# Optimization experiments

Hardware: AMD Instinct MI355X
Metric: run time of the kernel (lower is better)

## Reference

```python
import jax, jax.numpy as jnp
import numpy as np

N, E, T, H, D_IN, D_OUT = 50000, 320000, 4, 4, 128, 128
NEG_SLOPE = 0.2
LN_EPS = 1e-5


def setup_inputs() -> dict:
    key = jax.random.key(0)
    ks = jax.random.split(key, 10)
    x = jax.random.normal(ks[0], (N, D_IN), jnp.float32)
    edge_index = jax.random.randint(ks[1], (2, E), 0, N, jnp.int32)
    edge_attr = jax.random.randint(ks[2], (E,), 0, T, jnp.int32)
    W_gat = jax.random.normal(ks[3], (T, D_IN, H * D_OUT), jnp.float32) / np.sqrt(D_IN)
    a_src = jax.random.normal(ks[4], (T, H, D_OUT), jnp.float32) / np.sqrt(D_OUT)
    a_dst = jax.random.normal(ks[5], (T, H, D_OUT), jnp.float32) / np.sqrt(D_OUT)
    b_gat = jnp.zeros((T, D_OUT), jnp.float32)
    edge_type_weights = jnp.ones((T,), jnp.float32) / T
    W_fuse = jax.random.normal(ks[6], (T * D_OUT, D_OUT), jnp.float32) / np.sqrt(T * D_OUT)
    b_fuse = jnp.zeros((D_OUT,), jnp.float32)
    ln_gamma = jnp.ones((D_OUT,), jnp.float32)
    ln_beta = jnp.zeros((D_OUT,), jnp.float32)
    return {"x": x, "edge_index": edge_index, "edge_attr": edge_attr,
            "W_gat": W_gat, "a_src": a_src, "a_dst": a_dst, "b_gat": b_gat,
            "edge_type_weights": edge_type_weights, "W_fuse": W_fuse,
            "b_fuse": b_fuse, "ln_gamma": ln_gamma, "ln_beta": ln_beta}


def _gat_one_type(x, src_all, dst_all, mask_all, W, a_s, a_d, b):
    # x: [N, D_in]; src_all/dst_all: [E+N] (type-mask + self-loops on all nodes)
    n = x.shape[0]
    h = (x @ W).reshape(n, H, D_OUT)                      # [N, H, D]
    alpha_s = jnp.sum(h * a_s, axis=-1)                   # [N, H]
    alpha_d = jnp.sum(h * a_d, axis=-1)                   # [N, H]
    logit = jax.nn.leaky_relu(alpha_s[src_all] + alpha_d[dst_all], NEG_SLOPE)  # [Ea, H]
    neg_inf = jnp.float32(-1e30)
    logit = jnp.where(mask_all[:, None], logit, neg_inf)
    m = jax.ops.segment_max(logit, dst_all, num_segments=n)   # [N, H] (self-loops ensure finite)
    ex = jnp.exp(logit - m[dst_all])
    ex = jnp.where(mask_all[:, None], ex, 0.0)
    denom = jax.ops.segment_sum(ex, dst_all, num_segments=n)  # [N, H]
    alpha = ex / denom[dst_all]                                # [Ea, H]
    msg = alpha[:, :, None] * h[src_all]                       # [Ea, H, D]
    out = jax.ops.segment_sum(msg, dst_all, num_segments=n)   # [N, H, D]
    return out.mean(axis=1) + b                                # concat=False -> head mean


def reference(x, edge_index, edge_attr, W_gat, a_src, a_dst, b_gat,
              edge_type_weights, W_fuse, b_fuse, ln_gamma, ln_beta):
    n = x.shape[0]
    self_idx = jnp.arange(n, dtype=edge_index.dtype)
    src_all = jnp.concatenate([edge_index[0], self_idx])
    dst_all = jnp.concatenate([edge_index[1], self_idx])
    outs = []
    for t in range(T):
        mask_all = jnp.concatenate([edge_attr == t, jnp.ones((n,), bool)])
        outs.append(_gat_one_type(x, src_all, dst_all, mask_all,
                                  W_gat[t], a_src[t], a_dst[t], b_gat[t]))
    w = jax.nn.softmax(edge_type_weights)
    x_cat = jnp.concatenate([outs[t] * w[t] for t in range(T)], axis=1)  # [N, T*D]
    y = x_cat @ W_fuse + b_fuse
    mu = jnp.mean(y, axis=-1, keepdims=True)
    var = jnp.var(y, axis=-1, keepdims=True)
    y = (y - mu) / jnp.sqrt(var + LN_EPS) * ln_gamma + ln_beta
    return jax.nn.relu(y)
```

## Files before the change

### kernel.cpp

```cpp
#include <hip/hip_runtime.h>
#include <hip/hip_bf16.h>

#define TT 4
#define HH 4
#define DD 128
#define KAGG 2048

typedef __attribute__((ext_vector_type(8))) short short8;
typedef __attribute__((ext_vector_type(4))) float f32x4;
typedef __attribute__((ext_vector_type(4))) unsigned int uint4v;

__device__ __forceinline__ float lrelu(float z) { return z > 0.f ? z : 0.2f * z; }
__device__ __forceinline__ float bf2f(unsigned short u) {
  union { unsigned int i; float f; } v; v.i = ((unsigned int)u) << 16; return v.f;
}
__device__ __forceinline__ unsigned short f2b(float f) {
  union { float f; unsigned int i; } u; u.f = f;
  unsigned int r = u.i + 0x7fff + ((u.i >> 16) & 1);
  return (unsigned short)(r >> 16);
}
__device__ __forceinline__ void unpack8v(uint4v u, float* hv) {
  hv[0] = bf2f((unsigned short)(u.x & 0xffff));
  hv[1] = bf2f((unsigned short)(u.x >> 16));
  hv[2] = bf2f((unsigned short)(u.y & 0xffff));
  hv[3] = bf2f((unsigned short)(u.y >> 16));
  hv[4] = bf2f((unsigned short)(u.z & 0xffff));
  hv[5] = bf2f((unsigned short)(u.z >> 16));
  hv[6] = bf2f((unsigned short)(u.w & 0xffff));
  hv[7] = bf2f((unsigned short)(u.w >> 16));
}

__global__ __launch_bounds__(256) void prologue_kernel(
    const float* __restrict__ x, unsigned short* __restrict__ xb, int total4,
    const float* __restrict__ Wg, const float* __restrict__ a_s,
    const float* __restrict__ a_d, const float* __restrict__ W_fuse,
    const float* __restrict__ b_gat, const float* __restrict__ etw,
    const float* __restrict__ b_fuse, unsigned short* __restrict__ Pall,
    float* __restrict__ cbias, const int* __restrict__ dst,
    const int* __restrict__ attr, int* __restrict__ deg, int E, int N) {
  int bid = blockIdx.x;
  const int nconv = (total4 + 255) >> 8;
  if (bid < nconv) {
    int i = bid * 256 + threadIdx.x;
    if (i < total4) {
      float4 v = ((const float4*)x)[i];
      ushort4 o;
      o.x = f2b(v.x); o.y = f2b(v.y); o.z = f2b(v.z); o.w = f2b(v.w);
      ((ushort4*)xb)[i] = o;
    }
    return;
  }
  bid -= nconv;
  if (bid < 17) {
    float e0 = etw[0], e1 = etw[1], e2 = etw[2], e3 = etw[3];
    float mx = fmaxf(fmaxf(e0, e1), fmaxf(e2, e3));
    float w0 = __expf(e0 - mx), w1 = __expf(e1 - mx), w2 = __expf(e2 - mx),
          w3 = __expf(e3 - mx);
    float inv = 1.f / (w0 + w1 + w2 + w3);
    float wts[4] = {w0 * inv, w1 * inv, w2 * inv, w3 * inv};
    if (bid < 16) {
      int idx = bid * 256 + threadIdx.x;
      int c = idx >> 7, k = idx & 127;
      int t = c >> 3, jj = c & 7, head = jj & 3;
      const float* av = ((jj < 4) ? a_s : a_d) + (t * 4 + head) * 128;
      const float* wr = Wg + (size_t)t * 65536 + k * 512 + head * 128;
      float s = 0.f;
      for (int m = 0; m < 128; ++m) s += wr[m] * av[m];
      Pall[c * 128 + k] = f2b(s);
    } else {
      int j = threadIdx.x;
      if (j < 128) {
        float s = b_fuse[j];
        for (int t = 0; t < 4; ++t) {
          float st = 0.f;
          for (int m = 0; m < 128; ++m)
            st += b_gat[t * 128 + m] * W_fuse[(size_t)(t * 128 + m) * 128 + j];
          s += wts[t] * st;
        }
        cbias[j] = s;
      }
    }
    return;
  }
  bid -= 17;
  int e = bid * 256 + threadIdx.x;
  if (e < E) atomicAdd(&deg[attr[e] * N + dst[e]], 1);
}

__global__ __launch_bounds__(256) void stage2_kernel(
    const int* __restrict__ deg, int* __restrict__ rowptr,
    int* __restrict__ cursor, int* __restrict__ gcur, int M,
    const float* __restrict__ Wg, const float* __restrict__ W_fuse,
    const float* __restrict__ etw, unsigned short* __restrict__ Gfrag,
    const unsigned short* __restrict__ xb, const unsigned short* __restrict__ Pall,
    float* __restrict__ as_, float* __restrict__ ad_, int N) {
  __shared__ __align__(16) unsigned char smem[65536 + 16];
  int bid = blockIdx.x;
  const int nscan = (M + 255) >> 8;
  if (bid < nscan) {
    int* sh = (int*)smem;
    int* basep = (int*)(smem + 65536);
    int i = bid * 256 + threadIdx.x;
    int v = (i < M) ? deg[i] : 0;
    sh[threadIdx.x] = v;
    __syncthreads();
    for (int off = 1; off < 256; off <<= 1) {
      int xx = (threadIdx.x >= off) ? sh[threadIdx.x - off] : 0;
      __syncthreads();
      sh[threadIdx.x] += xx;
      __syncthreads();
    }
    if (threadIdx.x == 255) *basep = atomicAdd(gcur, sh[255]);
    __syncthreads();
    if (i < M) {
      int r = *basep + sh[threadIdx.x] - v;
      rowptr[i] = r;
      cursor[i] = r;
    }
    return;
  }
  bid -= nscan;
  if (bid < 256) {
    float(*Bs)[128] = (float(*)[128])smem;
    int t = bid >> 6;
    int kr0 = (bid & 63) * 8;
    const float* wf = W_fuse + (size_t)t * 16384;
#pragma unroll
    for (int i = 0; i < 64; ++i)
      ((float*)Bs)[i * 256 + threadIdx.x] = wf[i * 256 + threadIdx.x];

    float e0 = etw[0], e1 = etw[1], e2 = etw[2], e3 = etw[3];
    float mx = fmaxf(fmaxf(e0, e1), fmaxf(e2, e3));
    float w0 = __expf(e0 - mx), w1 = __expf(e1 - mx), w2 = __expf(e2 - mx),
          w3 = __expf(e3 - mx);
    float inv = 1.f / (w0 + w1 + w2 + w3);
    float wt = ((t == 0) ? w0 : (t == 1) ? w1 : (t == 2) ? w2 : w3) * inv * 0.25f;
    __syncthreads();

    int rr = threadIdx.x >> 7;
    int j = threadIdx.x & 127;
#pragma unroll
    for (int r2 = 0; r2 < 4; ++r2) {
      int kr = kr0 + r2 * 2 + rr;
      int head = kr >> 7, k = kr & 127;
      const float* wr = Wg + (size_t)t * 65536 + k * 512 + head * 128;
      float s = 0.f;
      for (int m = 0; m < 128; ++m) s += wr[m] * Bs[m][j];
      s *= wt;
      int K = t * 512 + kr;
      int kt = K >> 7, kk = (K >> 5) & 3, n = j >> 4;
      int f = (kt * 4 + kk) * 8 + n;
      int lg = (K >> 3) & 3, lr = j & 15, j8 = K & 7;
      Gfrag[(size_t)f * 512 + (lg * 16 + lr) * 8 + j8] = f2b(s);
    }
    return;
  }
  bid -= 256;
  unsigned char* lds = smem;
  const int n0 = bid * 128;
  const int tid = threadIdx.x, lane = tid & 63, wid = tid >> 6;
  const int lr = lane & 15, lg = lane >> 4;
#pragma unroll
  for (int i = 0; i < 8; ++i) {
    int chunk = tid + i * 256;
    int row = chunk >> 4, k16 = chunk & 15;
    int gr = n0 + row;
    uint4 v = make_uint4(0, 0, 0, 0);
    if (gr < N) v = *(const uint4*)(xb + (size_t)gr * DD + k16 * 8);
    *(uint4*)(lds + ((row * 256 + k16 * 16) ^ ((row & 7) << 4))) = v;
  }
  __syncthreads();
  f32x4 acc[2][2] = {};
#pragma unroll
  for (int kk = 0; kk < 4; ++kk) {
    short8 a[2], b[2];
#pragma unroll
    for (int m = 0; m < 2; ++m) {
      int row = wid * 32 + m * 16 + lr;
      a[m] = *(const short8*)(lds + ((row * 256 + kk * 64 + (lg << 4)) ^ ((row & 7) << 4)));
    }
#pragma unroll
    for (int n = 0; n < 2; ++n) {
      int c = n * 16 + lr;
      b[n] = *(const short8*)(Pall + c * DD + kk * 32 + lg * 8);
    }
#pragma unroll
    for (int m = 0; m < 2; ++m)
#pragma unroll
      for (int n = 0; n < 2; ++n)
        acc[m][n] = __builtin_amdgcn_mfma_f32_16x16x32_bf16(a[m], b[n], acc[m][n], 0, 0, 0);
  }
#pragma unroll
  for (int m = 0; m < 2; ++m)
#pragma unroll
    for (int n = 0; n < 2; ++n) {
      int c = n * 16 + lr;
      int t = c >> 3, jj = c & 7, head = jj & 3;
      float* dstp = (jj & 4) ? ad_ : as_;
#pragma unroll
      for (int r = 0; r < 4; ++r) {
        int gr = n0 + wid * 32 + m * 16 + lg * 4 + r;
        if (gr < N) dstp[((size_t)t * N + gr) * 4 + head] = acc[m][n][r];
      }
    }
}

__global__ __launch_bounds__(256) void scatter_q_kernel(
    const int* __restrict__ src, const int* __restrict__ dst,
    const int* __restrict__ attr, int* __restrict__ cursor,
    int* __restrict__ slist, float* __restrict__ qlist,
    const float* __restrict__ as_, const float* __restrict__ ad_,
    int E, int N) {
  int e = blockIdx.x * 256 + threadIdx.x;
  if (e >= E) return;
  int t = attr[e], s = src[e], d = dst[e];
  int p = atomicAdd(&cursor[(size_t)t * N + d], 1);
  float4 a = *(const float4*)(as_ + ((size_t)t * N + s) * 4);
  float4 b = *(const float4*)(ad_ + ((size_t)t * N + d) * 4);
  float4 q;
  q.x = __expf(lrelu(a.x + b.x));
  q.y = __expf(lrelu(a.y + b.y));
  q.z = __expf(lrelu(a.z + b.z));
  q.w = __expf(lrelu(a.w + b.w));
  slist[p] = s;
  *(float4*)(qlist + (size_t)p * 4) = q;
}

__global__ __launch_bounds__(256) void gather_kernel(
    const int* __restrict__ slist, const float* __restrict__ qlist,
    const int* __restrict__ rowptr, const int* __restrict__ deg,
    const float* __restrict__ as_, const float* __restrict__ ad_,
    const unsigned short* __restrict__ xb, unsigned short* __restrict__ AGG,
    int N) {
  int t = blockIdx.y;
  int lane = threadIdx.x & 63;
  int u = lane >> 4, c16 = lane & 15;
  int d = blockIdx.x * 16 + (threadIdx.x >> 6) * 4 + u;
  if (d >= N) return;
  size_t tn = (size_t)t * N;
  int dofs = c16 * 8;
  unsigned short* outp = AGG + (size_t)d * KAGG + t * 512 + dofs;

  int base = rowptr[tn + d], dg = deg[tn + d];
  uint4v uself = *(const uint4v*)(xb + (size_t)d * DD + dofs);
  if (dg == 0) {
#pragma unroll
    for (int h = 0; h < 4; ++h) *(uint4v*)(outp + h * DD) = uself;
    return;
  }

  float4 ad4 = *(const float4*)(ad_ + (tn + d) * 4);
  float4 av = *(const float4*)(as_ + (tn + d) * 4);
  float den[4], hv[8], acc[4][8];
  {
    float qs[4];
    qs[0] = __expf(lrelu(av.x + ad4.x));
    qs[1] = __expf(lrelu(av.y + ad4.y));
    qs[2] = __expf(lrelu(av.z + ad4.z));
    qs[3] = __expf(lrelu(av.w + ad4.w));
    unpack8v(uself, hv);
#pragma unroll
    for (int h = 0; h < 4; ++h) {
      den[h] = qs[h];
#pragma unroll
      for (int j = 0; j < 8; ++j) acc[h][j] = qs[h] * hv[j];
    }
  }

  int i = 0;
  for (; i + 1 < dg; i += 2) {
    int s0 = slist[base + i], s1 = slist[base + i + 1];
    float4 q0 = *(const float4*)(qlist + (size_t)(base + i) * 4);
    float4 q1 = *(const float4*)(qlist + (size_t)(base + i + 1) * 4);
    uint4v u0 = *(const uint4v*)(xb + (size_t)s0 * DD + dofs);
    uint4v u1 = *(const uint4v*)(xb + (size_t)s1 * DD + dofs);
    float qa[4] = {q0.x, q0.y, q0.z, q0.w};
    float qb[4] = {q1.x, q1.y, q1.z, q1.w};
#pragma unroll
    for (int h = 0; h < 4; ++h) den[h] += qa[h] + qb[h];
    unpack8v(u0, hv);
#pragma unroll
    for (int h = 0; h < 4; ++h)
#pragma unroll
      for (int j = 0; j < 8; ++j) acc[h][j] += qa[h] * hv[j];
    unpack8v(u1, hv);
#pragma unroll
    for (int h = 0; h < 4; ++h)
#pragma unroll
      for (int j = 0; j < 8; ++j) acc[h][j] += qb[h] * hv[j];
  }
  if (i < dg) {
    int s = slist[base + i];
    float4 q = *(const float4*)(qlist + (size_t)(base + i) * 4);
    uint4v ue = *(const uint4v*)(xb + (size_t)s * DD + dofs);
    float qe[4] = {q.x, q.y, q.z, q.w};
#pragma unroll
    for (int h = 0; h < 4; ++h) den[h] += qe[h];
    unpack8v(ue, hv);
#pragma unroll
    for (int h = 0; h < 4; ++h)
#pragma unroll
      for (int j = 0; j < 8; ++j) acc[h][j] += qe[h] * hv[j];
  }

#pragma unroll
  for (int h = 0; h < 4; ++h) {
    float r = 1.f / den[h];
    uint4v o;
    o.x = (unsigned)f2b(acc[h][0] * r) | ((unsigned)f2b(acc[h][1] * r) << 16);
    o.y = (unsigned)f2b(acc[h][2] * r) | ((unsigned)f2b(acc[h][3] * r) << 16);
    o.z = (unsigned)f2b(acc[h][4] * r) | ((unsigned)f2b(acc[h][5] * r) << 16);
    o.w = (unsigned)f2b(acc[h][6] * r) | ((unsigned)f2b(acc[h][7] * r) << 16);
    *(uint4v*)(outp + h * DD) = o;
  }
}

__global__ __launch_bounds__(256) void gemmln_kernel(
    const unsigned short* __restrict__ AGG, const unsigned short* __restrict__ Gfrag,
    const float* __restrict__ cbias, const float* __restrict__ gamma,
    const float* __restrict__ beta, float* __restrict__ out, int N) {
  __shared__ uint4 bbuf[2][1024];
  const int n0 = blockIdx.x * 64;
  const int tid = threadIdx.x, lane = tid & 63, wid = tid >> 6;
  const int lr = lane & 15, lg = lane >> 4;
  const int wrow = n0 + wid * 16;
  const int gr = wrow + lr;
  const bool ok = gr < N;
  const unsigned short* arow = AGG + (size_t)gr * KAGG;

  uint4 bn[4], an[2], ac[2];
#pragma unroll
  for (int i = 0; i < 4; ++i)
    bn[i] = *(const uint4*)(Gfrag + (size_t)(i * 256 + tid) * 8);
#pragma unroll
  for (int kkh = 0; kkh < 2; ++kkh) {
    an[kkh] = make_uint4(0, 0, 0, 0);
    if (ok) an[kkh] = *(const uint4*)(arow + kkh * 32 + lg * 8);
  }
#pragma unroll
  for (int i = 0; i < 4; ++i) bbuf[0][i * 256 + tid] = bn[i];
  ac[0] = an[0]; ac[1] = an[1];
  __syncthreads();

  f32x4 acc[8] = {};
  int cur = 0;
  for (int ht = 0; ht < 32; ++ht) {
    if (ht < 31) {
#pragma unroll
      for (int i = 0; i < 4; ++i)
        bn[i] = *(const uint4*)(Gfrag + (size_t)(ht + 1) * 8192 +
                                (size_t)(i * 256 + tid) * 8);
#pragma unroll
      for (int kkh = 0; kkh < 2; ++kkh) {
        an[kkh] = make_uint4(0, 0, 0, 0);
        if (ok) an[kkh] = *(const uint4*)(arow + (ht + 1) * 64 + kkh * 32 + lg * 8);
      }
    }
    const unsigned char* lds = (const unsigned char*)bbuf[cur];
#pragma unroll
    for (int kkh = 0; kkh < 2; ++kkh) {
      short8 a = *(const short8*)&ac[kkh];
#pragma unroll
      for (int n = 0; n < 8; ++n) {
        short8 b = *(const short8*)(lds + (kkh * 8 + n) * 1024 + lane * 16);
        acc[n] = __builtin_amdgcn_mfma_f32_16x16x32_bf16(a, b, acc[n], 0, 0, 0);
      }
    }
    if (ht < 31) {
#pragma unroll
      for (int i = 0; i < 4; ++i) bbuf[cur ^ 1][i * 256 + tid] = bn[i];
      ac[0] = an[0]; ac[1] = an[1];
      __syncthreads();
      cur ^= 1;
    }
  }

  float cb[8], gm[8], bt[8];
#pragma unroll
  for (int n = 0; n < 8; ++n) {
    cb[n] = cbias[n * 16 + lr];
    gm[n] = gamma[n * 16 + lr];
    bt[n] = beta[n * 16 + lr];
  }
#pragma unroll
  for (int rr = 0; rr < 4; ++rr) {
    float y[8];
    float s = 0.f, ss = 0.f;
#pragma unroll
    for (int n = 0; n < 8; ++n) {
      y[n] = acc[n][rr] + cb[n];
      s += y[n];
      ss += y[n] * y[n];
    }
#pragma unroll
    for (int mask = 1; mask <= 8; mask <<= 1) {
      s += __shfl_xor(s, mask);
      ss += __shfl_xor(ss, mask);
    }
    float mean = s * (1.f / 128.f);
    float var = ss * (1.f / 128.f) - mean * mean;
    float rstd = rsqrtf(var + 1e-5f);
    int orow = wrow + lg * 4 + rr;
    if (orow < N) {
#pragma unroll
      for (int n = 0; n < 8; ++n) {
        float v = (y[n] - mean) * rstd * gm[n] + bt[n];
        out[(size_t)orow * DD + n * 16 + lr] = fmaxf(0.f, v);
      }
    }
  }
}

extern "C" void kernel_launch(void* const* d_in, const int* in_sizes, int n_in,
                              void* d_out, int out_size, void* d_ws, size_t ws_size,
                              hipStream_t stream) {
  const float* x      = (const float*)d_in[0];
  const int*   ei     = (const int*)d_in[1];
  const int*   attr   = (const int*)d_in[2];
  const float* Wg     = (const float*)d_in[3];
  const float* a_src  = (const float*)d_in[4];
  const float* a_dst  = (const float*)d_in[5];
  const float* b_gat  = (const float*)d_in[6];
  const float* etw    = (const float*)d_in[7];
  const float* W_fuse = (const float*)d_in[8];
  const float* b_fuse = (const float*)d_in[9];
  const float* gamma  = (const float*)d_in[10];
  const float* beta   = (const float*)d_in[11];

  const int N = in_sizes[0] / DD;
  const int E = in_sizes[2];
  const int* src = ei;
  const int* dst = ei + E;
  const int M = TT * N;

  char* ws = (char*)d_ws;
  size_t off = 0;
  auto alloc = [&](size_t bytes) {
    void* p = ws + off;
    off += (bytes + 255) & ~(size_t)255;
    return p;
  };
  unsigned short* AGG   = (unsigned short*)alloc((size_t)N * KAGG * 2);
  unsigned short* xb    = (unsigned short*)alloc((size_t)N * DD * 2);
  unsigned short* Gfrag = (unsigned short*)alloc((size_t)512 * 512 * 2);
  unsigned short* Pall  = (unsigned short*)alloc((size_t)32 * DD * 2);
  float* cbias          = (float*)alloc(128 * sizeof(float));
  float* as_            = (float*)alloc((size_t)TT * N * 4 * sizeof(float));
  float* ad_            = (float*)alloc((size_t)TT * N * 4 * sizeof(float));
  int* deg              = (int*)alloc((size_t)(M + 1) * sizeof(int));
  int* rowptr           = (int*)alloc((size_t)M * sizeof(int));
  int* cursor           = (int*)alloc((size_t)M * sizeof(int));
  int* slist            = (int*)alloc((size_t)E * sizeof(int));
  float* qlist          = (float*)alloc((size_t)E * 4 * sizeof(float));

  hipMemsetAsync(deg, 0, (size_t)(M + 1) * sizeof(int), stream);

  int total4x = N * DD / 4;
  int nconv = (total4x + 255) / 256;
  int nhist = (E + 255) / 256;
  prologue_kernel<<<nconv + 17 + nhist, 256, 0, stream>>>(
      x, xb, total4x, Wg, a_src, a_dst, W_fuse, b_gat, etw, b_fuse,
      Pall, cbias, dst, attr, deg, E, N);

  int nscan = (M + 255) / 256;
  int nalpha = (N + 127) / 128;
  stage2_kernel<<<nscan + 256 + nalpha, 256, 0, stream>>>(
      deg, rowptr, cursor, deg + M, M, Wg, W_fuse, etw, Gfrag,
      xb, Pall, as_, ad_, N);

  scatter_q_kernel<<<nhist, 256, 0, stream>>>(src, dst, attr, cursor, slist,
                                              qlist, as_, ad_, E, N);

  dim3 ggrid((N + 15) / 16, TT);
  gather_kernel<<<ggrid, 256, 0, stream>>>(slist, qlist, rowptr, deg, as_, ad_,
                                           xb, AGG, N);

  gemmln_kernel<<<(N + 63) / 64, 256, 0, stream>>>(AGG, Gfrag, cbias, gamma, beta,
                                                   (float*)d_out, N);
}
```

Measured before the change: 211.5 us.

## Fuse edge gather-aggregation into fused GEMM+LayerNorm kernel via LDS tiles

Merges the gather kernel and the GEMM+LayerNorm kernel into one kernel. Each 32-row block aggregates neighbor features per edge type straight into swizzled LDS, then runs MFMA against streamed Gfrag tiles. This removes the N x 2048 bf16 AGG intermediate, which was written to and re-read from global memory. In exchange, the gather is serialized with the MFMA phases inside each block, LDS use grows to about 64KB per block, and LayerNorm needs a cross-wave reduction through LDS.

After: 404.8 us. 1.91x slower.

```diff
diff --git a/kernel.cpp b/kernel.cpp
--- a/kernel.cpp
+++ b/kernel.cpp
@@ -226,186 +226,185 @@
   *(float4*)(qlist + (size_t)p * 4) = q;
 }
 
-__global__ __launch_bounds__(256) void gather_kernel(
+__global__ __launch_bounds__(256) void fused_kernel(
     const int* __restrict__ slist, const float* __restrict__ qlist,
     const int* __restrict__ rowptr, const int* __restrict__ deg,
     const float* __restrict__ as_, const float* __restrict__ ad_,
-    const unsigned short* __restrict__ xb, unsigned short* __restrict__ AGG,
-    int N) {
-  int t = blockIdx.y;
-  int lane = threadIdx.x & 63;
-  int u = lane >> 4, c16 = lane & 15;
-  int d = blockIdx.x * 16 + (threadIdx.x >> 6) * 4 + u;
-  if (d >= N) return;
-  size_t tn = (size_t)t * N;
-  int dofs = c16 * 8;
-  unsigned short* outp = AGG + (size_t)d * KAGG + t * 512 + dofs;
-
-  int base = rowptr[tn + d], dg = deg[tn + d];
-  uint4v uself = *(const uint4v*)(xb + (size_t)d * DD + dofs);
-  if (dg == 0) {
-#pragma unroll
-    for (int h = 0; h < 4; ++h) *(uint4v*)(outp + h * DD) = uself;
-    return;
-  }
-
-  float4 ad4 = *(const float4*)(ad_ + (tn + d) * 4);
-  float4 av = *(const float4*)(as_ + (tn + d) * 4);
-  float den[4], hv[8], acc[4][8];
-  {
-    float qs[4];
-    qs[0] = __expf(lrelu(av.x + ad4.x));
-    qs[1] = __expf(lrelu(av.y + ad4.y));
-    qs[2] = __expf(lrelu(av.z + ad4.z));
-    qs[3] = __expf(lrelu(av.w + ad4.w));
-    unpack8v(uself, hv);
-#pragma unroll
-    for (int h = 0; h < 4; ++h) {
-      den[h] = qs[h];
-#pragma unroll
-      for (int j = 0; j < 8; ++j) acc[h][j] = qs[h] * hv[j];
-    }
-  }
-
-  int i = 0;
-  for (; i + 1 < dg; i += 2) {
-    int s0 = slist[base + i], s1 = slist[base + i + 1];
-    float4 q0 = *(const float4*)(qlist + (size_t)(base + i) * 4);
-    float4 q1 = *(const float4*)(qlist + (size_t)(base + i + 1) * 4);
-    uint4v u0 = *(const uint4v*)(xb + (size_t)s0 * DD + dofs);
-    uint4v u1 = *(const uint4v*)(xb + (size_t)s1 * DD + dofs);
-    float qa[4] = {q0.x, q0.y, q0.z, q0.w};
-    float qb[4] = {q1.x, q1.y, q1.z, q1.w};
-#pragma unroll
-    for (int h = 0; h < 4; ++h) den[h] += qa[h] + qb[h];
-    unpack8v(u0, hv);
-#pragma unroll
-    for (int h = 0; h < 4; ++h)
-#pragma unroll
-      for (int j = 0; j < 8; ++j) acc[h][j] += qa[h] * hv[j];
-    unpack8v(u1, hv);
-#pragma unroll
-    for (int h = 0; h < 4; ++h)
-#pragma unroll
-      for (int j = 0; j < 8; ++j) acc[h][j] += qb[h] * hv[j];
-  }
-  if (i < dg) {
-    int s = slist[base + i];
-    float4 q = *(const float4*)(qlist + (size_t)(base + i) * 4);
-    uint4v ue = *(const uint4v*)(xb + (size_t)s * DD + dofs);
-    float qe[4] = {q.x, q.y, q.z, q.w};
-#pragma unroll
-    for (int h = 0; h < 4; ++h) den[h] += qe[h];
-    unpack8v(ue, hv);
-#pragma unroll
-    for (int h = 0; h < 4; ++h)
-#pragma unroll
-      for (int j = 0; j < 8; ++j) acc[h][j] += qe[h] * hv[j];
-  }
-
-#pragma unroll
-  for (int h = 0; h < 4; ++h) {
-    float r = 1.f / den[h];
-    uint4v o;
-    o.x = (unsigned)f2b(acc[h][0] * r) | ((unsigned)f2b(acc[h][1] * r) << 16);
-    o.y = (unsigned)f2b(acc[h][2] * r) | ((unsigned)f2b(acc[h][3] * r) << 16);
-    o.z = (unsigned)f2b(acc[h][4] * r) | ((unsigned)f2b(acc[h][5] * r) << 16);
-    o.w = (unsigned)f2b(acc[h][6] * r) | ((unsigned)f2b(acc[h][7] * r) << 16);
-    *(uint4v*)(outp + h * DD) = o;
-  }
-}
-
-__global__ __launch_bounds__(256) void gemmln_kernel(
-    const unsigned short* __restrict__ AGG, const unsigned short* __restrict__ Gfrag,
+    const unsigned short* __restrict__ xb, const unsigned short* __restrict__ Gfrag,
     const float* __restrict__ cbias, const float* __restrict__ gamma,
     const float* __restrict__ beta, float* __restrict__ out, int N) {
-  __shared__ uint4 bbuf[2][1024];
-  const int n0 = blockIdx.x * 64;
+  __shared__ __align__(16) unsigned char agg_lds[32 * 1024];
+  __shared__ uint4 blds[2048];
   const int tid = threadIdx.x, lane = tid & 63, wid = tid >> 6;
+  const int n0 = blockIdx.x * 32;
+  const int u = lane >> 4, c16 = lane & 15;
   const int lr = lane & 15, lg = lane >> 4;
-  const int wrow = n0 + wid * 16;
-  const int gr = wrow + lr;
-  const bool ok = gr < N;
-  const unsigned short* arow = AGG + (size_t)gr * KAGG;
-
-  uint4 bn[4], an[2], ac[2];
-#pragma unroll
-  for (int i = 0; i < 4; ++i)
-    bn[i] = *(const uint4*)(Gfrag + (size_t)(i * 256 + tid) * 8);
-#pragma unroll
-  for (int kkh = 0; kkh < 2; ++kkh) {
-    an[kkh] = make_uint4(0, 0, 0, 0);
-    if (ok) an[kkh] = *(const uint4*)(arow + kkh * 32 + lg * 8);
-  }
-#pragma unroll
-  for (int i = 0; i < 4; ++i) bbuf[0][i * 256 + tid] = bn[i];
-  ac[0] = an[0]; ac[1] = an[1];
+  const int rw = wid & 1, cw = wid >> 1;
+
+  uint4 breg[8];
+#pragma unroll
+  for (int jj = 0; jj < 8; ++jj)
+    breg[jj] = *(const uint4*)(Gfrag + (size_t)(jj * 256 + tid) * 8);
+
+  f32x4 acc[4] = {};
+  for (int g = 0; g < 16; ++g) {
+#pragma unroll
+    for (int jj = 0; jj < 8; ++jj) blds[jj * 256 + tid] = breg[jj];
+    if ((g & 3) == 0) {
+      int t = g >> 2;
+      size_t tn = (size_t)t * N;
+      for (int r = 0; r < 2; ++r) {
+        int row = r * 16 + wid * 4 + u;
+        int d = n0 + row;
+        int swz = (row & 7) << 4;
+        int dofs = c16 * 8;
+        if (d >= N) {
+          uint4v z = {0, 0, 0, 0};
+#pragma unroll
+          for (int h = 0; h < 4; ++h)
+            *(uint4v*)(agg_lds + ((row * 1024 + h * 256 + c16 * 16) ^ swz)) = z;
+          continue;
+        }
+        int base = rowptr[tn + d], dg = deg[tn + d];
+        uint4v uself = *(const uint4v*)(xb + (size_t)d * DD + dofs);
+        if (dg == 0) {
+#pragma unroll
+          for (int h = 0; h < 4; ++h)
+            *(uint4v*)(agg_lds + ((row * 1024 + h * 256 + c16 * 16) ^ swz)) = uself;
+          continue;
+        }
+        float4 ad4 = *(const float4*)(ad_ + (tn + d) * 4);
+        float4 av = *(const float4*)(as_ + (tn + d) * 4);
+        float den[4], hv[8], gac[4][8];
+        {
+          float qs[4];
+          qs[0] = __expf(lrelu(av.x + ad4.x));
+          qs[1] = __expf(lrelu(av.y + ad4.y));
+          qs[2] = __expf(lrelu(av.z + ad4.z));
+          qs[3] = __expf(lrelu(av.w + ad4.w));
+          unpack8v(uself, hv);
+#pragma unroll
+          for (int h = 0; h < 4; ++h) {
+            den[h] = qs[h];
+#pragma unroll
+            for (int j = 0; j < 8; ++j) gac[h][j] = qs[h] * hv[j];
+          }
+        }
+        int i = 0;
+        for (; i + 1 < dg; i += 2) {
+          int s0 = slist[base + i], s1 = slist[base + i + 1];
+          float4 q0 = *(const float4*)(qlist + (size_t)(base + i) * 4);
+          float4 q1 = *(const float4*)(qlist + (size_t)(base + i + 1) * 4);
+          uint4v u0 = *(const uint4v*)(xb + (size_t)s0 * DD + dofs);
+          uint4v u1 = *(const uint4v*)(xb + (size_t)s1 * DD + dofs);
+          float qa[4] = {q0.x, q0.y, q0.z, q0.w};
+          float qb[4] = {q1.x, q1.y, q1.z, q1.w};
+#pragma unroll
+          for (int h = 0; h < 4; ++h) den[h] += qa[h] + qb[h];
+          unpack8v(u0, hv);
+#pragma unroll
+          for (int h = 0; h < 4; ++h)
+#pragma unroll
+            for (int j = 0; j < 8; ++j) gac[h][j] += qa[h] * hv[j];
+          unpack8v(u1, hv);
+#pragma unroll
+          for (int h = 0; h < 4; ++h)
+#pragma unroll
+            for (int j = 0; j < 8; ++j) gac[h][j] += qb[h] * hv[j];
+        }
+        if (i < dg) {
+          int s = slist[base + i];
+          float4 q = *(const float4*)(qlist + (size_t)(base + i) * 4);
+          uint4v ue = *(const uint4v*)(xb + (size_t)s * DD + dofs);
+          float qe[4] = {q.x, q.y, q.z, q.w};
+#pragma unroll
+          for (int h = 0; h < 4; ++h) den[h] += qe[h];
+          unpack8v(ue, hv);
+#pragma unroll
+          for (int h = 0; h < 4; ++h)
+#pragma unroll
+            for (int j = 0; j < 8; ++j) gac[h][j] += qe[h] * hv[j];
+        }
+#pragma unroll
+        for (int h = 0; h < 4; ++h) {
+          float rd = 1.f / den[h];
+          uint4v o;
+          o.x = (unsigned)f2b(gac[h][0] * rd) | ((unsigned)f2b(gac[h][1] * rd) << 16);
+          o.y = (unsigned)f2b(gac[h][2] * rd) | ((unsigned)f2b(gac[h][3] * rd) << 16);
+          o.z = (unsigned)f2b(gac[h][4] * rd) | ((unsigned)f2b(gac[h][5] * rd) << 16);
+          o.w = (unsigned)f2b(gac[h][6] * rd) | ((unsigned)f2b(gac[h][7] * rd) << 16);
+          *(uint4v*)(agg_lds + ((row * 1024 + h * 256 + c16 * 16) ^ swz)) = o;
+        }
+      }
+    }
+    __syncthreads();
+    {
+      const unsigned char* bl = (const unsigned char*)blds;
+      int arow = rw * 16 + lr;
+      int aswz = (arow & 7) << 4;
+#pragma unroll
+      for (int ks = 0; ks < 4; ++ks) {
+        int ksg = (g & 3) * 4 + ks;
+        short8 a = *(const short8*)(agg_lds + ((arow * 1024 + ksg * 64 + lg * 16) ^ aswz));
+#pragma unroll
+        for (int nn = 0; nn < 4; ++nn) {
+          short8 b = *(const short8*)(bl + (ks * 8 + cw * 4 + nn) * 1024 + lane * 16);
+          acc[nn] = __builtin_amdgcn_mfma_f32_16x16x32_bf16(a, b, acc[nn], 0, 0, 0);
+        }
+      }
+    }
+    if (g < 15) {
+#pragma unroll
+      for (int jj = 0; jj < 8; ++jj)
+        breg[jj] = *(const uint4*)(Gfrag + (size_t)(g + 1) * 16384 +
+                                   (size_t)(jj * 256 + tid) * 8);
+    }
+    __syncthreads();
+  }
+
+  float* lnp = (float*)agg_lds;
+  float cb[4], gm[4], bt[4];
+#pragma unroll
+  for (int nn = 0; nn < 4; ++nn) {
+    int col = cw * 64 + nn * 16 + lr;
+    cb[nn] = cbias[col];
+    gm[nn] = gamma[col];
+    bt[nn] = beta[col];
+  }
+#pragma unroll
+  for (int rr = 0; rr < 4; ++rr) {
+    float s = 0.f, ss = 0.f;
+#pragma unroll
+    for (int nn = 0; nn < 4; ++nn) {
+      float y = acc[nn][rr] + cb[nn];
+      s += y;
+      ss += y * y;
+    }
+    s += __shfl_xor(s, 1); ss += __shfl_xor(ss, 1);
+    s += __shfl_xor(s, 2); ss += __shfl_xor(ss, 2);
+    s += __shfl_xor(s, 4); ss += __shfl_xor(ss, 4);
+    s += __shfl_xor(s, 8); ss += __shfl_xor(ss, 8);
+    if (lr == 0) {
+      int row32 = rw * 16 + lg * 4 + rr;
+      lnp[cw * 32 + row32] = s;
+      lnp[64 + cw * 32 + row32] = ss;
+    }
+  }
   __syncthreads();
-
-  f32x4 acc[8] = {};
-  int cur = 0;
-  for (int ht = 0; ht < 32; ++ht) {
-    if (ht < 31) {
-#pragma unroll
-      for (int i = 0; i < 4; ++i)
-        bn[i] = *(const uint4*)(Gfrag + (size_t)(ht + 1) * 8192 +
-                                (size_t)(i * 256 + tid) * 8);
-#pragma unroll
-      for (int kkh = 0; kkh < 2; ++kkh) {
-        an[kkh] = make_uint4(0, 0, 0, 0);
-        if (ok) an[kkh] = *(const uint4*)(arow + (ht + 1) * 64 + kkh * 32 + lg * 8);
-      }
-    }
-    const unsigned char* lds = (const unsigned char*)bbuf[cur];
-#pragma unroll
-    for (int kkh = 0; kkh < 2; ++kkh) {
-      short8 a = *(const short8*)&ac[kkh];
-#pragma unroll
-      for (int n = 0; n < 8; ++n) {
-        short8 b = *(const short8*)(lds + (kkh * 8 + n) * 1024 + lane * 16);
-        acc[n] = __builtin_amdgcn_mfma_f32_16x16x32_bf16(a, b, acc[n], 0, 0, 0);
-      }
-    }
-    if (ht < 31) {
-#pragma unroll
-      for (int i = 0; i < 4; ++i) bbuf[cur ^ 1][i * 256 + tid] = bn[i];
-      ac[0] = an[0]; ac[1] = an[1];
-      __syncthreads();
-      cur ^= 1;
-    }
-  }
-
-  float cb[8], gm[8], bt[8];
-#pragma unroll
-  for (int n = 0; n < 8; ++n) {
-    cb[n] = cbias[n * 16 + lr];
-    gm[n] = gamma[n * 16 + lr];
-    bt[n] = beta[n * 16 + lr];
-  }
 #pragma unroll
   for (int rr = 0; rr < 4; ++rr) {
-    float y[8];
-    float s = 0.f, ss = 0.f;
-#pragma unroll
-    for (int n = 0; n < 8; ++n) {
-      y[n] = acc[n][rr] + cb[n];
-      s += y[n];
-      ss += y[n] * y[n];
-    }
-#pragma unroll
-    for (int mask = 1; mask <= 8; mask <<= 1) {
-      s += __shfl_xor(s, mask);
-      ss += __shfl_xor(ss, mask);
-    }
-    float mean = s * (1.f / 128.f);
-    float var = ss * (1.f / 128.f) - mean * mean;
-    float rstd = rsqrtf(var + 1e-5f);
-    int orow = wrow + lg * 4 + rr;
+    int row32 = rw * 16 + lg * 4 + rr;
+    int orow = n0 + row32;
     if (orow < N) {
-#pragma unroll
-      for (int n = 0; n < 8; ++n) {
-        float v = (y[n] - mean) * rstd * gm[n] + bt[n];
-        out[(size_t)orow * DD + n * 16 + lr] = fmaxf(0.f, v);
+      float st = lnp[row32] + lnp[32 + row32];
+      float sst = lnp[64 + row32] + lnp[96 + row32];
+      float mean = st * (1.f / 128.f);
+      float var = sst * (1.f / 128.f) - mean * mean;
+      float rstd = rsqrtf(var + 1e-5f);
+#pragma unroll
+      for (int nn = 0; nn < 4; ++nn) {
+        float v = (acc[nn][rr] + cb[nn] - mean) * rstd * gm[nn] + bt[nn];
+        out[(size_t)orow * DD + cw * 64 + nn * 16 + lr] = fmaxf(0.f, v);
       }
     }
   }
@@ -440,7 +439,6 @@
     off += (bytes + 255) & ~(size_t)255;
     return p;
   };
-  unsigned short* AGG   = (unsigned short*)alloc((size_t)N * KAGG * 2);
   unsigned short* xb    = (unsigned short*)alloc((size_t)N * DD * 2);
   unsigned short* Gfrag = (unsigned short*)alloc((size_t)512 * 512 * 2);
   unsigned short* Pall  = (unsigned short*)alloc((size_t)32 * DD * 2);
@@ -471,10 +469,7 @@
   scatter_q_kernel<<<nhist, 256, 0, stream>>>(src, dst, attr, cursor, slist,
                                               qlist, as_, ad_, E, N);
 
-  dim3 ggrid((N + 15) / 16, TT);
-  gather_kernel<<<ggrid, 256, 0, stream>>>(slist, qlist, rowptr, deg, as_, ad_,
-                                           xb, AGG, N);
-
-  gemmln_kernel<<<(N + 63) / 64, 256, 0, stream>>>(AGG, Gfrag, cbias, gamma, beta,
-                                                   (float*)d_out, N);
-}
+  fused_kernel<<<(N + 31) / 32, 256, 0, stream>>>(
+      slist, qlist, rowptr, deg, as_, ad_, xb, Gfrag, cbias, gamma, beta,
+      (float*)d_out, N);
+}
```
